# Kernel optimization log

Hardware: AMD Instinct MI355X
Metric: run time of the kernel (lower is better)

Reference implementation:

```python
import jax, jax.numpy as jnp
import numpy as np

BSZ, DIM, SEQ_A, SEQ_B = 16, 768, 1024, 1024


def setup_inputs() -> dict:
    key = jax.random.key(0)
    kA, kB, kU = jax.random.split(key, 3)
    input_A = jax.random.normal(kA, (BSZ, DIM, SEQ_A), dtype=jnp.float32)
    input_B = jax.random.normal(kB, (BSZ, DIM, SEQ_B), dtype=jnp.float32)
    intput_msk = jnp.zeros((BSZ, SEQ_A, SEQ_B), dtype=jnp.float32)  # 0 = on, -inf = off
    U = jax.random.normal(kU, (DIM, DIM), dtype=jnp.float32)
    return {"input_A": input_A, "input_B": input_B, "intput_msk": intput_msk, "U": U}


def reference(input_A, input_B, intput_msk, U):
    # align[b,s,t] = tanh( A[b,:,s]^T U B[b,:,t] )  -> (bsz, seq_A, seq_B)
    align = jnp.einsum("bds,de,bet->bst", input_A, U, input_B)
    align = jnp.tanh(align) + intput_msk
    # per-token scores: max over the other modality's sequence, then softmax
    score_A = jax.nn.softmax(jnp.max(align, axis=2), axis=-1)  # (bsz, seq_A)
    score_B = jax.nn.softmax(jnp.max(align, axis=1), axis=-1)  # (bsz, seq_B)
    output_A = jnp.einsum("bds,bs->bd", input_A, score_A)  # (bsz, dim_A)
    output_B = jnp.einsum("bdt,bt->bd", input_B, score_B)  # (bsz, dim_B)
    return (output_A, output_B)
```

## Files before the change

kernel.cpp:

```cpp
#include <hip/hip_runtime.h>
#include <math.h>

#define BSZ  16
#define DIM  768
#define SEQA 1024
#define SEQB 1024

typedef float f32x4 __attribute__((ext_vector_type(4)));
typedef long long llong;

__device__ inline void gload_lds16(const void* g, void* l) {
    __builtin_amdgcn_global_load_lds(
        (const __attribute__((address_space(1))) void*)g,
        (__attribute__((address_space(3))) void*)l, 16, 0, 0);
}

__device__ inline unsigned enc_key(float f) {
    unsigned u = __float_as_uint(f);
    return (u & 0x80000000u) ? ~u : (u | 0x80000000u);
}
__device__ inline float dec_key(unsigned k) {
    return (k & 0x80000000u) ? __uint_as_float(k ^ 0x80000000u) : __uint_as_float(~k);
}

__device__ inline unsigned pk4_fp8(float a, float b, float c, float d) {
    int v = 0;
    v = __builtin_amdgcn_cvt_pk_fp8_f32(a, b, v, false);
    v = __builtin_amdgcn_cvt_pk_fp8_f32(c, d, v, true);
    return (unsigned)v;
}
__device__ inline unsigned char f2fp8(float a) {
    return (unsigned char)(__builtin_amdgcn_cvt_pk_fp8_f32(a, a, 0, false) & 0xFF);
}

__device__ inline float fast_tanh(float x) {
    float ax = fabsf(x);
    float u = __expf(-2.0f * ax);
    float th = __fdividef(1.0f - u, 1.0f + u);
    return copysignf(th, x);
}

__global__ __launch_bounds__(256) void t_cast_AB(const float* __restrict__ A,
                                                 const float* __restrict__ B,
                                                 unsigned char* __restrict__ At,
                                                 unsigned char* __restrict__ Bt) {
    __shared__ float tl[64][68];
    const int z = blockIdx.z;
    const float* X = (z < BSZ) ? A : B;
    unsigned char* Y = (z < BSZ) ? At : Bt;
    const int b = z & 15;
    const int d0 = blockIdx.y * 64;
    const int s0 = blockIdx.x * 64;
    const int tid = threadIdx.x;
    const int rr = tid >> 4, c4 = tid & 15;
    const float* Xb = X + ((size_t)b * DIM + d0) * SEQA + s0;
#pragma unroll
    for (int i = 0; i < 4; i++) {
        int row = i * 16 + rr;
        float4 v = *(const float4*)&Xb[(size_t)row * SEQA + c4 * 4];
        *(float4*)&tl[row][c4 * 4] = v;
    }
    __syncthreads();
    unsigned char* Yb = Y + ((size_t)b * SEQA + s0) * DIM + d0;
    const int m = tid & 15, sl = tid >> 4;
#pragma unroll
    for (int i = 0; i < 4; i++) {
        int s = sl + 16 * i;
        unsigned v = pk4_fp8(tl[4 * m + 0][s], tl[4 * m + 1][s], tl[4 * m + 2][s], tl[4 * m + 3][s]);
        *(unsigned*)&Yb[(size_t)s * DIM + 4 * m] = v;
    }
}

__global__ __launch_bounds__(256) void t_cast_U(const float* __restrict__ U,
                                                unsigned char* __restrict__ Ut,
                                                unsigned* __restrict__ keyA,
                                                unsigned* __restrict__ keyB) {
    __shared__ float tl[64][68];
    const int d0 = blockIdx.y * 64;
    const int e0 = blockIdx.x * 64;
    const int tid = threadIdx.x;
    const int bid = blockIdx.y * gridDim.x + blockIdx.x;
    if (bid < 64) {
        int i = bid * 256 + tid;
        keyA[i] = 0u;
        keyB[i] = 0u;
    }
    const int rr = tid >> 4, c4 = tid & 15;
#pragma unroll
    for (int i = 0; i < 4; i++) {
        int row = i * 16 + rr;
        float4 v = *(const float4*)&U[(size_t)(d0 + row) * DIM + e0 + c4 * 4];
        *(float4*)&tl[row][c4 * 4] = v;
    }
    __syncthreads();
    const int m = tid & 15, sl = tid >> 4;
#pragma unroll
    for (int i = 0; i < 4; i++) {
        int e = sl + 16 * i;
        unsigned v = pk4_fp8(tl[4 * m + 0][e], tl[4 * m + 1][e], tl[4 * m + 2][e], tl[4 * m + 3][e]);
        *(unsigned*)&Ut[(size_t)(e0 + e) * DIM + d0 + 4 * m] = v;
    }
}

__device__ inline void stage_tile(const unsigned char* __restrict__ src, int row0,
                                  int kbyte0, unsigned char* lds, int wid, int lane) {
    const int r8 = lane >> 3;
    const int g  = lane & 7;
    const int gg = g ^ (r8 & 7);
#pragma unroll
    for (int t = 0; t < 4; ++t) {
        int row = row0 + wid * 32 + t * 8 + r8;
        gload_lds16(src + (size_t)row * DIM + kbyte0 + gg * 16,
                    lds + (wid * 32 + t * 8) * 128 + lane * 16);
    }
}

__device__ inline llong frag_read(const unsigned char* lds, int rowbase, int l15,
                                  int quad, int h) {
    int gg = 2 * h + (quad >> 1);
    int off = (rowbase + l15) * 128 + ((gg ^ (l15 & 7)) << 4) + (quad & 1) * 8;
    return *(const llong*)(lds + off);
}

__global__ __launch_bounds__(256) void k1_ua(const unsigned char* __restrict__ At,
                                             const unsigned char* __restrict__ Ut,
                                             unsigned char* __restrict__ Ct) {
    __shared__ __align__(16) unsigned char As[128 * 128];
    __shared__ __align__(16) unsigned char Us[128 * 128];
    const int b  = blockIdx.z;
    const int s0 = blockIdx.x * 128;
    const int e0 = blockIdx.y * 128;
    const int tid = threadIdx.x;
    const int lane = tid & 63;
    const int wid = tid >> 6;
    const int wr = wid >> 1, wc = wid & 1;
    const int quad = lane >> 4, l15 = lane & 15;

    const unsigned char* Atb = At + (size_t)b * SEQA * DIM;
    f32x4 acc[4][4] = {};

    for (int d0 = 0; d0 < DIM; d0 += 128) {
        stage_tile(Atb + (size_t)s0 * DIM, 0, d0, As, wid, lane);
        stage_tile(Ut + (size_t)e0 * DIM, 0, d0, Us, wid, lane);
        __syncthreads();
#pragma unroll
        for (int h = 0; h < 4; ++h) {
            llong av[4], bv[4];
#pragma unroll
            for (int i = 0; i < 4; ++i) av[i] = frag_read(As, wr * 64 + 16 * i, l15, quad, h);
#pragma unroll
            for (int j = 0; j < 4; ++j) bv[j] = frag_read(Us, wc * 64 + 16 * j, l15, quad, h);
#pragma unroll
            for (int i = 0; i < 4; ++i)
#pragma unroll
                for (int j = 0; j < 4; ++j)
                    acc[i][j] = __builtin_amdgcn_mfma_f32_16x16x32_fp8_fp8(av[i], bv[j], acc[i][j], 0, 0, 0);
        }
        __syncthreads();
    }
    unsigned char* Cb = Ct + (size_t)b * SEQA * DIM;
#pragma unroll
    for (int i = 0; i < 4; ++i)
#pragma unroll
        for (int j = 0; j < 4; ++j) {
            int e_g = e0 + wc * 64 + 16 * j + l15;
#pragma unroll
            for (int r = 0; r < 4; ++r) {
                int s_g = s0 + wr * 64 + 16 * i + quad * 4 + r;
                Cb[(size_t)s_g * DIM + e_g] = f2fp8(acc[i][j][r]);
            }
        }
}

__global__ __launch_bounds__(256, 2) void k2_align(const unsigned char* __restrict__ Ct,
                                                   const unsigned char* __restrict__ Bt,
                                                   const float* __restrict__ msk,
                                                   unsigned* __restrict__ keyA,
                                                   unsigned* __restrict__ keyB) {
    __shared__ __align__(16) unsigned char Cs[128 * 128];
    __shared__ __align__(16) unsigned char Bs[128 * 128];
    const int b  = blockIdx.z;
    const int t0 = blockIdx.x * 128;
    const int s0 = blockIdx.y * 128;
    const int tid = threadIdx.x;
    const int lane = tid & 63;
    const int wid = tid >> 6;
    const int wr = wid >> 1, wc = wid & 1;
    const int quad = lane >> 4, l15 = lane & 15;

    const float* Mb = msk + (size_t)b * SEQA * SEQB;
    float4 mv[4][4];
#pragma unroll
    for (int i = 0; i < 4; ++i)
#pragma unroll
        for (int j = 0; j < 4; ++j) {
            int s_g = s0 + wc * 64 + 16 * j + l15;
            int t_g = t0 + wr * 64 + 16 * i + quad * 4;
            mv[i][j] = *(const float4*)&Mb[(size_t)s_g * SEQB + t_g];
        }

    f32x4 acc[4][4] = {};

    for (int e0 = 0; e0 < DIM; e0 += 128) {
        stage_tile(Ct + (size_t)(b * SEQA + s0) * DIM, 0, e0, Cs, wid, lane);
        stage_tile(Bt + (size_t)(b * SEQB + t0) * DIM, 0, e0, Bs, wid, lane);
        __syncthreads();
#pragma unroll
        for (int h = 0; h < 4; ++h) {
            llong av[4], bv[4];
#pragma unroll
            for (int i = 0; i < 4; ++i) av[i] = frag_read(Bs, wr * 64 + 16 * i, l15, quad, h);
#pragma unroll
            for (int j = 0; j < 4; ++j) bv[j] = frag_read(Cs, wc * 64 + 16 * j, l15, quad, h);
#pragma unroll
            for (int i = 0; i < 4; ++i)
#pragma unroll
                for (int j = 0; j < 4; ++j)
                    acc[i][j] = __builtin_amdgcn_mfma_f32_16x16x32_fp8_fp8(av[i], bv[j], acc[i][j], 0, 0, 0);
        }
        __syncthreads();
    }

#pragma unroll
    for (int i = 0; i < 4; ++i)
#pragma unroll
        for (int j = 0; j < 4; ++j) {
            acc[i][j][0] = fast_tanh(acc[i][j][0]) + mv[i][j].x;
            acc[i][j][1] = fast_tanh(acc[i][j][1]) + mv[i][j].y;
            acc[i][j][2] = fast_tanh(acc[i][j][2]) + mv[i][j].z;
            acc[i][j][3] = fast_tanh(acc[i][j][3]) + mv[i][j].w;
        }
#pragma unroll
    for (int j = 0; j < 4; ++j) {
        float m = -INFINITY;
#pragma unroll
        for (int i = 0; i < 4; ++i)
#pragma unroll
            for (int r = 0; r < 4; ++r) m = fmaxf(m, acc[i][j][r]);
        m = fmaxf(m, __shfl_xor(m, 16));
        m = fmaxf(m, __shfl_xor(m, 32));
        if (quad == 0)
            atomicMax(&keyA[b * SEQA + s0 + wc * 64 + 16 * j + l15], enc_key(m));
    }
#pragma unroll
    for (int i = 0; i < 4; ++i)
#pragma unroll
        for (int r = 0; r < 4; ++r) {
            float m = fmaxf(fmaxf(acc[i][0][r], acc[i][1][r]), fmaxf(acc[i][2][r], acc[i][3][r]));
            m = fmaxf(m, __shfl_xor(m, 1));
            m = fmaxf(m, __shfl_xor(m, 2));
            m = fmaxf(m, __shfl_xor(m, 4));
            m = fmaxf(m, __shfl_xor(m, 8));
            if (l15 == 0)
                atomicMax(&keyB[b * SEQB + t0 + wr * 64 + 16 * i + quad * 4 + r], enc_key(m));
        }
}

__global__ __launch_bounds__(256) void k3_softmax(const unsigned* __restrict__ keyA,
                                                  const unsigned* __restrict__ keyB,
                                                  float* __restrict__ scoreA,
                                                  float* __restrict__ scoreB) {
    const int b = blockIdx.x;
    const bool isA = (blockIdx.y == 0);
    const unsigned* keys = isA ? (keyA + b * SEQA) : (keyB + b * SEQB);
    float* score = isA ? (scoreA + b * SEQA) : (scoreB + b * SEQB);
    __shared__ float sh[4];
    const int tid = threadIdx.x;
    float m[4];
    float mx = -INFINITY;
#pragma unroll
    for (int k = 0; k < 4; k++) {
        m[k] = dec_key(keys[tid + 256 * k]);
        mx = fmaxf(mx, m[k]);
    }
#pragma unroll
    for (int o = 32; o > 0; o >>= 1) mx = fmaxf(mx, __shfl_down(mx, o, 64));
    if ((tid & 63) == 0) sh[tid >> 6] = mx;
    __syncthreads();
    mx = fmaxf(fmaxf(sh[0], sh[1]), fmaxf(sh[2], sh[3]));
    __syncthreads();
    float e[4];
    float sum = 0.f;
#pragma unroll
    for (int k = 0; k < 4; k++) { e[k] = expf(m[k] - mx); sum += e[k]; }
#pragma unroll
    for (int o = 32; o > 0; o >>= 1) sum += __shfl_down(sum, o, 64);
    if ((tid & 63) == 0) sh[tid >> 6] = sum;
    __syncthreads();
    sum = sh[0] + sh[1] + sh[2] + sh[3];
    float inv = 1.0f / sum;
#pragma unroll
    for (int k = 0; k < 4; k++) score[tid + 256 * k] = e[k] * inv;
}

__global__ __launch_bounds__(256) void k4_out(const float* __restrict__ A,
                                              const float* __restrict__ B,
                                              const float* __restrict__ scoreA,
                                              const float* __restrict__ scoreB,
                                              float* __restrict__ out) {
    const int which = blockIdx.y;
    const int row = blockIdx.x * 4 + (threadIdx.x >> 6);
    const int lane = threadIdx.x & 63;
    const float* X = which ? B : A;
    const float* S = which ? scoreB : scoreA;
    const int b = row / DIM;
    const float4* xr = (const float4*)(X + (size_t)row * SEQA);
    const float4* sr = (const float4*)(S + (size_t)b * SEQA);
    float acc = 0.f;
#pragma unroll
    for (int q = lane; q < SEQA / 4; q += 64) {
        float4 x = xr[q];
        float4 s = sr[q];
        acc += x.x * s.x + x.y * s.y + x.z * s.z + x.w * s.w;
    }
#pragma unroll
    for (int o = 32; o > 0; o >>= 1) acc += __shfl_down(acc, o, 64);
    if (lane == 0) out[which * (BSZ * DIM) + row] = acc;
}

extern "C" void kernel_launch(void* const* d_in, const int* in_sizes, int n_in,
                              void* d_out, int out_size, void* d_ws, size_t ws_size,
                              hipStream_t stream) {
    const float* A   = (const float*)d_in[0];
    const float* B   = (const float*)d_in[1];
    const float* msk = (const float*)d_in[2];
    const float* U   = (const float*)d_in[3];
    float* out = (float*)d_out;

    char* ws = (char*)d_ws;
    unsigned char* At = (unsigned char*)ws;
    unsigned char* Bt = (unsigned char*)(ws + 12582912);
    unsigned char* Ct = (unsigned char*)(ws + 25165824);
    unsigned char* Ut = (unsigned char*)(ws + 37748736);
    unsigned* keyA   = (unsigned*)(ws + 38338560);
    unsigned* keyB   = (unsigned*)(ws + 38404096);
    float*    scoreA = (float*)   (ws + 38469632);
    float*    scoreB = (float*)   (ws + 38535168);

    t_cast_U<<<dim3(DIM / 64, DIM / 64, 1), 256, 0, stream>>>(U, Ut, keyA, keyB);
    t_cast_AB<<<dim3(SEQA / 64, DIM / 64, 2 * BSZ), 256, 0, stream>>>(A, B, At, Bt);
    k1_ua<<<dim3(SEQA / 128, DIM / 128, BSZ), 256, 0, stream>>>(At, Ut, Ct);
    k2_align<<<dim3(SEQB / 128, SEQA / 128, BSZ), 256, 0, stream>>>(Ct, Bt, msk, keyA, keyB);
    k3_softmax<<<dim3(BSZ, 2), 256, 0, stream>>>(keyA, keyB, scoreA, scoreB);
    k4_out<<<dim3(BSZ * DIM / 4, 2), 256, 0, stream>>>(A, B, scoreA, scoreB, out);
}
```

Baseline: 245.9 us.

## Double-buffer GEMM K-loop and add bf16 transposed copy for output reduction

The k1 and k2 GEMM kernels now stage 64-wide K slices into two LDS buffers, so the next slice loads while the current one computes. k2 also drops its occupancy hint and loads the mask only after the GEMM, which should cut register pressure. When the workspace is large enough, the cast kernel also writes a bf16 transposed copy of A and B. A new k4 kernel then reduces over that copy with atomics after a memset, replacing the fp32 read of A and B. This trades extra write traffic and lower output precision for a cheaper final reduction.

```diff
diff --git a/kernel.cpp b/kernel.cpp
--- a/kernel.cpp
+++ b/kernel.cpp
@@ -32,6 +32,13 @@
 __device__ inline unsigned char f2fp8(float a) {
     return (unsigned char)(__builtin_amdgcn_cvt_pk_fp8_f32(a, a, 0, false) & 0xFF);
 }
+__device__ inline unsigned short f2bf(float f) {
+    unsigned u = __float_as_uint(f);
+    return (unsigned short)((u + 0x7FFF + ((u >> 16) & 1)) >> 16);
+}
+__device__ inline float bf2f(unsigned short h) {
+    return __uint_as_float((unsigned)h << 16);
+}
 
 __device__ inline float fast_tanh(float x) {
     float ax = fabsf(x);
@@ -43,11 +50,15 @@
 __global__ __launch_bounds__(256) void t_cast_AB(const float* __restrict__ A,
                                                  const float* __restrict__ B,
                                                  unsigned char* __restrict__ At,
-                                                 unsigned char* __restrict__ Bt) {
+                                                 unsigned char* __restrict__ Bt,
+                                                 unsigned short* __restrict__ At16,
+                                                 unsigned short* __restrict__ Bt16,
+                                                 int w16) {
     __shared__ float tl[64][68];
     const int z = blockIdx.z;
     const float* X = (z < BSZ) ? A : B;
     unsigned char* Y = (z < BSZ) ? At : Bt;
+    unsigned short* Y16 = (z < BSZ) ? At16 : Bt16;
     const int b = z & 15;
     const int d0 = blockIdx.y * 64;
     const int s0 = blockIdx.x * 64;
@@ -61,13 +72,24 @@
         *(float4*)&tl[row][c4 * 4] = v;
     }
     __syncthreads();
+    const int m = tid & 15, sl = tid >> 4;
     unsigned char* Yb = Y + ((size_t)b * SEQA + s0) * DIM + d0;
-    const int m = tid & 15, sl = tid >> 4;
 #pragma unroll
     for (int i = 0; i < 4; i++) {
         int s = sl + 16 * i;
         unsigned v = pk4_fp8(tl[4 * m + 0][s], tl[4 * m + 1][s], tl[4 * m + 2][s], tl[4 * m + 3][s]);
         *(unsigned*)&Yb[(size_t)s * DIM + 4 * m] = v;
+    }
+    if (w16) {
+        unsigned short* Yc = Y16 + ((size_t)b * SEQA + s0) * DIM + d0;
+#pragma unroll
+        for (int i = 0; i < 4; i++) {
+            int s = sl + 16 * i;
+            uint2 w;
+            w.x = (unsigned)f2bf(tl[4 * m + 0][s]) | ((unsigned)f2bf(tl[4 * m + 1][s]) << 16);
+            w.y = (unsigned)f2bf(tl[4 * m + 2][s]) | ((unsigned)f2bf(tl[4 * m + 3][s]) << 16);
+            *(uint2*)&Yc[(size_t)s * DIM + 4 * m] = w;
+        }
     }
 }
 
@@ -102,31 +124,28 @@
     }
 }
 
-__device__ inline void stage_tile(const unsigned char* __restrict__ src, int row0,
-                                  int kbyte0, unsigned char* lds, int wid, int lane) {
-    const int r8 = lane >> 3;
-    const int g  = lane & 7;
-    const int gg = g ^ (r8 & 7);
-#pragma unroll
-    for (int t = 0; t < 4; ++t) {
-        int row = row0 + wid * 32 + t * 8 + r8;
-        gload_lds16(src + (size_t)row * DIM + kbyte0 + gg * 16,
-                    lds + (wid * 32 + t * 8) * 128 + lane * 16);
-    }
-}
-
-__device__ inline llong frag_read(const unsigned char* lds, int rowbase, int l15,
-                                  int quad, int h) {
-    int gg = 2 * h + (quad >> 1);
-    int off = (rowbase + l15) * 128 + ((gg ^ (l15 & 7)) << 4) + (quad & 1) * 8;
-    return *(const llong*)(lds + off);
-}
+__device__ inline void stage64(const unsigned char* __restrict__ src, int kbyte0,
+                               unsigned char* buf, int wid, int lane) {
+    const int grow = lane >> 1;
+    const int gcol = ((lane & 1) ^ ((lane >> 3) & 1)) * 16;
+#pragma unroll
+    for (int h = 0; h < 2; ++h)
+        gload_lds16(src + (size_t)(wid * 32 + grow) * DIM + kbyte0 + 32 * h + gcol,
+                    buf + h * 4096 + wid * 1024 + lane * 16);
+}
+__device__ inline llong frag64(const unsigned char* buf, int rowbase, int l15,
+                               int quad, int h) {
+    int koff = (((quad >> 1) ^ ((l15 >> 2) & 1)) << 4) + (quad & 1) * 8;
+    return *(const llong*)(buf + h * 4096 + (rowbase + l15) * 32 + koff);
+}
+
+#define NK (DIM / 64)
 
 __global__ __launch_bounds__(256) void k1_ua(const unsigned char* __restrict__ At,
                                              const unsigned char* __restrict__ Ut,
                                              unsigned char* __restrict__ Ct) {
-    __shared__ __align__(16) unsigned char As[128 * 128];
-    __shared__ __align__(16) unsigned char Us[128 * 128];
+    __shared__ __align__(16) unsigned char As[2][8192];
+    __shared__ __align__(16) unsigned char Us[2][8192];
     const int b  = blockIdx.z;
     const int s0 = blockIdx.x * 128;
     const int e0 = blockIdx.y * 128;
@@ -136,26 +155,38 @@
     const int wr = wid >> 1, wc = wid & 1;
     const int quad = lane >> 4, l15 = lane & 15;
 
-    const unsigned char* Atb = At + (size_t)b * SEQA * DIM;
+    const unsigned char* Ab = At + (size_t)(b * SEQA + s0) * DIM;
+    const unsigned char* Ub = Ut + (size_t)e0 * DIM;
     f32x4 acc[4][4] = {};
 
-    for (int d0 = 0; d0 < DIM; d0 += 128) {
-        stage_tile(Atb + (size_t)s0 * DIM, 0, d0, As, wid, lane);
-        stage_tile(Ut + (size_t)e0 * DIM, 0, d0, Us, wid, lane);
+#define K_COMPUTE(BUF)                                                               \
+    {                                                                                \
+        _Pragma("unroll") for (int h = 0; h < 2; ++h) {                              \
+            llong av[4], bv[4];                                                      \
+            _Pragma("unroll") for (int i = 0; i < 4; ++i)                            \
+                av[i] = frag64(As[BUF], wr * 64 + 16 * i, l15, quad, h);             \
+            _Pragma("unroll") for (int j = 0; j < 4; ++j)                            \
+                bv[j] = frag64(Us[BUF], wc * 64 + 16 * j, l15, quad, h);             \
+            _Pragma("unroll") for (int i = 0; i < 4; ++i)                            \
+                _Pragma("unroll") for (int j = 0; j < 4; ++j)                        \
+                    acc[i][j] = __builtin_amdgcn_mfma_f32_16x16x32_fp8_fp8(          \
+                        av[i], bv[j], acc[i][j], 0, 0, 0);                           \
+        }                                                                            \
+    }
+
+    stage64(Ab, 0, As[0], wid, lane);
+    stage64(Ub, 0, Us[0], wid, lane);
+    __syncthreads();
+    for (int it = 0; it < NK; it += 2) {
+        stage64(Ab, (it + 1) * 64, As[1], wid, lane);
+        stage64(Ub, (it + 1) * 64, Us[1], wid, lane);
+        K_COMPUTE(0);
         __syncthreads();
-#pragma unroll
-        for (int h = 0; h < 4; ++h) {
-            llong av[4], bv[4];
-#pragma unroll
-            for (int i = 0; i < 4; ++i) av[i] = frag_read(As, wr * 64 + 16 * i, l15, quad, h);
-#pragma unroll
-            for (int j = 0; j < 4; ++j) bv[j] = frag_read(Us, wc * 64 + 16 * j, l15, quad, h);
-#pragma unroll
-            for (int i = 0; i < 4; ++i)
-#pragma unroll
-                for (int j = 0; j < 4; ++j)
-                    acc[i][j] = __builtin_amdgcn_mfma_f32_16x16x32_fp8_fp8(av[i], bv[j], acc[i][j], 0, 0, 0);
-        }
+        if (it + 2 < NK) {
+            stage64(Ab, (it + 2) * 64, As[0], wid, lane);
+            stage64(Ub, (it + 2) * 64, Us[0], wid, lane);
+        }
+        K_COMPUTE(1);
         __syncthreads();
     }
     unsigned char* Cb = Ct + (size_t)b * SEQA * DIM;
@@ -172,13 +203,13 @@
         }
 }
 
-__global__ __launch_bounds__(256, 2) void k2_align(const unsigned char* __restrict__ Ct,
-                                                   const unsigned char* __restrict__ Bt,
-                                                   const float* __restrict__ msk,
-                                                   unsigned* __restrict__ keyA,
-                                                   unsigned* __restrict__ keyB) {
-    __shared__ __align__(16) unsigned char Cs[128 * 128];
-    __shared__ __align__(16) unsigned char Bs[128 * 128];
+__global__ __launch_bounds__(256) void k2_align(const unsigned char* __restrict__ Ct,
+                                                const unsigned char* __restrict__ Bt,
+                                                const float* __restrict__ msk,
+                                                unsigned* __restrict__ keyA,
+                                                unsigned* __restrict__ keyB) {
+    __shared__ __align__(16) unsigned char As[2][8192];
+    __shared__ __align__(16) unsigned char Us[2][8192];
     const int b  = blockIdx.z;
     const int t0 = blockIdx.x * 128;
     const int s0 = blockIdx.y * 128;
@@ -188,47 +219,38 @@
     const int wr = wid >> 1, wc = wid & 1;
     const int quad = lane >> 4, l15 = lane & 15;
 
+    const unsigned char* Bb = Bt + (size_t)(b * SEQB + t0) * DIM;
+    const unsigned char* Cb = Ct + (size_t)(b * SEQA + s0) * DIM;
+    f32x4 acc[4][4] = {};
+
+    stage64(Bb, 0, As[0], wid, lane);
+    stage64(Cb, 0, Us[0], wid, lane);
+    __syncthreads();
+    for (int it = 0; it < NK; it += 2) {
+        stage64(Bb, (it + 1) * 64, As[1], wid, lane);
+        stage64(Cb, (it + 1) * 64, Us[1], wid, lane);
+        K_COMPUTE(0);
+        __syncthreads();
+        if (it + 2 < NK) {
+            stage64(Bb, (it + 2) * 64, As[0], wid, lane);
+            stage64(Cb, (it + 2) * 64, Us[0], wid, lane);
+        }
+        K_COMPUTE(1);
+        __syncthreads();
+    }
+
     const float* Mb = msk + (size_t)b * SEQA * SEQB;
-    float4 mv[4][4];
 #pragma unroll
     for (int i = 0; i < 4; ++i)
 #pragma unroll
         for (int j = 0; j < 4; ++j) {
             int s_g = s0 + wc * 64 + 16 * j + l15;
             int t_g = t0 + wr * 64 + 16 * i + quad * 4;
-            mv[i][j] = *(const float4*)&Mb[(size_t)s_g * SEQB + t_g];
-        }
-
-    f32x4 acc[4][4] = {};
-
-    for (int e0 = 0; e0 < DIM; e0 += 128) {
-        stage_tile(Ct + (size_t)(b * SEQA + s0) * DIM, 0, e0, Cs, wid, lane);
-        stage_tile(Bt + (size_t)(b * SEQB + t0) * DIM, 0, e0, Bs, wid, lane);
-        __syncthreads();
-#pragma unroll
-        for (int h = 0; h < 4; ++h) {
-            llong av[4], bv[4];
-#pragma unroll
-            for (int i = 0; i < 4; ++i) av[i] = frag_read(Bs, wr * 64 + 16 * i, l15, quad, h);
-#pragma unroll
-            for (int j = 0; j < 4; ++j) bv[j] = frag_read(Cs, wc * 64 + 16 * j, l15, quad, h);
-#pragma unroll
-            for (int i = 0; i < 4; ++i)
-#pragma unroll
-                for (int j = 0; j < 4; ++j)
-                    acc[i][j] = __builtin_amdgcn_mfma_f32_16x16x32_fp8_fp8(av[i], bv[j], acc[i][j], 0, 0, 0);
-        }
-        __syncthreads();
-    }
-
-#pragma unroll
-    for (int i = 0; i < 4; ++i)
-#pragma unroll
-        for (int j = 0; j < 4; ++j) {
-            acc[i][j][0] = fast_tanh(acc[i][j][0]) + mv[i][j].x;
-            acc[i][j][1] = fast_tanh(acc[i][j][1]) + mv[i][j].y;
-            acc[i][j][2] = fast_tanh(acc[i][j][2]) + mv[i][j].z;
-            acc[i][j][3] = fast_tanh(acc[i][j][3]) + mv[i][j].w;
+            float4 mv = *(const float4*)&Mb[(size_t)s_g * SEQB + t_g];
+            acc[i][j][0] = fast_tanh(acc[i][j][0]) + mv.x;
+            acc[i][j][1] = fast_tanh(acc[i][j][1]) + mv.y;
+            acc[i][j][2] = fast_tanh(acc[i][j][2]) + mv.z;
+            acc[i][j][3] = fast_tanh(acc[i][j][3]) + mv.w;
         }
 #pragma unroll
     for (int j = 0; j < 4; ++j) {
@@ -293,7 +315,36 @@
     for (int k = 0; k < 4; k++) score[tid + 256 * k] = e[k] * inv;
 }
 
-__global__ __launch_bounds__(256) void k4_out(const float* __restrict__ A,
+__global__ __launch_bounds__(256) void k4_bf16(const unsigned short* __restrict__ At16,
+                                               const unsigned short* __restrict__ Bt16,
+                                               const float* __restrict__ scoreA,
+                                               const float* __restrict__ scoreB,
+                                               float* __restrict__ out) {
+    const int sc = blockIdx.x;
+    const int which = blockIdx.y;
+    const int b = blockIdx.z;
+    const unsigned short* X = which ? Bt16 : At16;
+    const float* S = which ? scoreB : scoreA;
+    __shared__ float sh[128];
+    const int tid = threadIdx.x;
+    if (tid < 128) sh[tid] = S[b * SEQA + sc * 128 + tid];
+    __syncthreads();
+    const unsigned short* Xb = X + ((size_t)b * SEQA + sc * 128) * DIM;
+    float a0 = 0.f, a1 = 0.f, a2 = 0.f;
+    for (int s = 0; s < 128; ++s) {
+        float f = sh[s];
+        const unsigned short* row = Xb + (size_t)s * DIM;
+        a0 += f * bf2f(row[tid]);
+        a1 += f * bf2f(row[tid + 256]);
+        a2 += f * bf2f(row[tid + 512]);
+    }
+    float* o = out + which * (BSZ * DIM) + b * DIM;
+    atomicAdd(&o[tid], a0);
+    atomicAdd(&o[tid + 256], a1);
+    atomicAdd(&o[tid + 512], a2);
+}
+
+__global__ __launch_bounds__(256) void k4_f32(const float* __restrict__ A,
                                               const float* __restrict__ B,
                                               const float* __restrict__ scoreA,
                                               const float* __restrict__ scoreB,
@@ -336,11 +387,19 @@
     unsigned* keyB   = (unsigned*)(ws + 38404096);
     float*    scoreA = (float*)   (ws + 38469632);
     float*    scoreB = (float*)   (ws + 38535168);
+    unsigned short* At16 = (unsigned short*)(ws + 38600704);
+    unsigned short* Bt16 = (unsigned short*)(ws + 63766528);
+    const int w16 = (ws_size >= 88932352ull) ? 1 : 0;
 
     t_cast_U<<<dim3(DIM / 64, DIM / 64, 1), 256, 0, stream>>>(U, Ut, keyA, keyB);
-    t_cast_AB<<<dim3(SEQA / 64, DIM / 64, 2 * BSZ), 256, 0, stream>>>(A, B, At, Bt);
+    t_cast_AB<<<dim3(SEQA / 64, DIM / 64, 2 * BSZ), 256, 0, stream>>>(A, B, At, Bt, At16, Bt16, w16);
     k1_ua<<<dim3(SEQA / 128, DIM / 128, BSZ), 256, 0, stream>>>(At, Ut, Ct);
     k2_align<<<dim3(SEQB / 128, SEQA / 128, BSZ), 256, 0, stream>>>(Ct, Bt, msk, keyA, keyB);
     k3_softmax<<<dim3(BSZ, 2), 256, 0, stream>>>(keyA, keyB, scoreA, scoreB);
-    k4_out<<<dim3(BSZ * DIM / 4, 2), 256, 0, stream>>>(A, B, scoreA, scoreB, out);
-}
+    if (w16) {
+        hipMemsetAsync(d_out, 0, (size_t)out_size * sizeof(float), stream);
+        k4_bf16<<<dim3(8, 2, BSZ), 256, 0, stream>>>(At16, Bt16, scoreA, scoreB, out);
+    } else {
+        k4_f32<<<dim3(BSZ * DIM / 4, 2), 256, 0, stream>>>(A, B, scoreA, scoreB, out);
+    }
+}
```

Measured after the change: 256.7 us. +4.4%, slower.
